# Kernel tuning notes

Measured on AMD Instinct MI355X. Metric: run time of the kernel, lower is better.

Reference implementation:

```python
import jax, jax.numpy as jnp
import numpy as np
import math

HEAD_DIM = 64
HEAD_NUM = 8  # hidden_dim(512) // head_dim(64)
EPS = 1e-8


def modulated_linear(x, s, weight, aff_w, aff_b):
    # x: [B, N, IN], s: [B, S], weight: [OUT, IN], aff_w: [IN, S], aff_b: [IN]
    style = s @ aff_w.T + aff_b                       # [B, IN]
    w = weight[None, :, :] * style[:, None, :]        # [B, OUT, IN]
    demod = jax.lax.rsqrt(jnp.sum(w * w, axis=2) + EPS)  # [B, OUT]
    w = w * demod[:, :, None]
    return jnp.einsum('bni,boi->bno', x, w)           # [B, N, OUT]


def setup_inputs() -> dict:
    key = jax.random.key(0)
    ks = jax.random.split(key, 8)
    B, N, F, S = 8, 1024, 512, 512
    sc = 1.0 / math.sqrt(F)
    return {
        'x': jax.random.normal(ks[0], (B, N, F), dtype=jnp.float32),
        's': jax.random.normal(ks[1], (B, S), dtype=jnp.float32),
        'k_weight': jax.random.normal(ks[2], (F, F), dtype=jnp.float32) * sc,
        'k_aff_w': jax.random.normal(ks[3], (F, S), dtype=jnp.float32) * sc,
        'k_aff_b': jnp.ones((F,), dtype=jnp.float32),
        'o_weight': jax.random.normal(ks[4], (F, F), dtype=jnp.float32) * sc,
        'o_aff_w': jax.random.normal(ks[5], (F, S), dtype=jnp.float32) * sc,
        'o_aff_b': jnp.ones((F,), dtype=jnp.float32),
    }


def reference(x, s, k_weight, k_aff_w, k_aff_b, o_weight, o_aff_w, o_aff_b):
    B, N, _ = x.shape
    # Original code computes q, k, v all via k_mapping (faithful to the bug).
    kqv = modulated_linear(x, s, k_weight, k_aff_w, k_aff_b)  # [B, N, hidden]
    kqv = kqv.reshape(B, N, HEAD_NUM, HEAD_DIM)               # [B, N, H, D]
    q = k = v = kqv
    scale = 1.0 / math.sqrt(HEAD_DIM)
    scores = jnp.einsum('bnhd,bmhd->bhnm', q, k) * scale      # [B, H, N, N]
    attn = jax.nn.softmax(scores, axis=-1)
    out = jnp.einsum('bhnm,bmhd->bnhd', attn, v)              # [B, N, H, D]
    out = out.reshape(B, N, HEAD_NUM * HEAD_DIM)
    return modulated_linear(out, s, o_weight, o_aff_w, o_aff_b)
```

## Files before the change

### kernel.cpp

```cpp
#include <hip/hip_runtime.h>
#include <stdint.h>

using short8  = __attribute__((ext_vector_type(8))) short;
using f32x4   = __attribute__((ext_vector_type(4))) float;
using float4v = __attribute__((ext_vector_type(4))) float;
using u16x4   = __attribute__((ext_vector_type(4))) unsigned short;

__device__ __forceinline__ unsigned short f2b(float f) {
    union { float f; unsigned int i; } v; v.f = f;
    unsigned int i = v.i;
    unsigned int r = (i + 0x7fffu + ((i >> 16) & 1u)) >> 16;
    return (unsigned short)r;
}
__device__ __forceinline__ short8 ld8(const unsigned short* p) {
    return *reinterpret_cast<const short8*>(p);
}
__device__ __forceinline__ void st8(unsigned short* p, short8 v) {
    *reinterpret_cast<short8*>(p) = v;
}
__device__ __forceinline__ short8 ldA(const unsigned short* p) { return ld8(p); }
__device__ __forceinline__ short8 ldA(const float* p) {
    float4v v0 = *reinterpret_cast<const float4v*>(p);
    float4v v1 = *reinterpret_cast<const float4v*>(p + 4);
    short8 o;
#pragma unroll
    for (int j = 0; j < 4; ++j) o[j] = (short)f2b(v0[j]);
#pragma unroll
    for (int j = 0; j < 4; ++j) o[4 + j] = (short)f2b(v1[j]);
    return o;
}
__device__ __forceinline__ f32x4 mfma16(short8 a, short8 b, f32x4 c) {
    return __builtin_amdgcn_mfma_f32_16x16x32_bf16(a, b, c, 0, 0, 0);
}
__device__ __forceinline__ void stC(float* p, float v)          { *p = v; }
__device__ __forceinline__ void stC(unsigned short* p, float v) { *p = f2b(v); }

__device__ __forceinline__ unsigned int cvtpk(float lo, float hi) {
    unsigned int r;
    asm("v_cvt_pk_bf16_f32 %0, %1, %2" : "=v"(r) : "v"(lo), "v"(hi));
    return r;
}
__device__ __forceinline__ void pl32swap(unsigned int& a, unsigned int& b) {
    asm("v_permlane32_swap_b32 %0, %1" : "+v"(a), "+v"(b));
}
__device__ __forceinline__ void pl16swap(unsigned int& a, unsigned int& b) {
    asm("v_permlane16_swap_b32 %0, %1" : "+v"(a), "+v"(b));
}
__device__ __forceinline__ short8 pack4(unsigned int x0, unsigned int x1,
                                        unsigned int x2, unsigned int x3) {
    union { unsigned int u[4]; short8 s; } c;
    c.u[0] = x0; c.u[1] = x1; c.u[2] = x2; c.u[3] = x3;
    return c.s;
}

__global__ __launch_bounds__(256) void style_kernel(
    const float* __restrict__ s,
    const float* __restrict__ k_aff_w, const float* __restrict__ k_aff_b,
    const float* __restrict__ o_aff_w, const float* __restrict__ o_aff_b,
    float* __restrict__ style)
{
    int wid  = blockIdx.x * 4 + (threadIdx.x >> 6);
    int lane = threadIdx.x & 63;
    int map  = wid >> 12;
    int rem  = wid & 4095;
    int b    = rem >> 9;
    int i    = rem & 511;
    const float* aw = map ? o_aff_w : k_aff_w;
    const float* ab = map ? o_aff_b : k_aff_b;
    const float* sp = s  + b * 512 + lane * 8;
    const float* wp = aw + i * 512 + lane * 8;
    float acc = 0.f;
#pragma unroll
    for (int j = 0; j < 8; ++j) acc += sp[j] * wp[j];
#pragma unroll
    for (int off = 1; off < 64; off <<= 1) acc += __shfl_xor(acc, off, 64);
    if (lane == 0) style[(map * 8 + b) * 512 + i] = acc + ab[i];
}

__global__ __launch_bounds__(256) void modw_kernel(
    const float* __restrict__ k_weight,
    const float* __restrict__ o_weight,
    const float* __restrict__ style,
    unsigned short* __restrict__ wmod)
{
    int wid  = blockIdx.x * 4 + (threadIdx.x >> 6);
    int lane = threadIdx.x & 63;
    int map  = wid >> 12;
    int rem  = wid & 4095;
    int b    = rem >> 9;
    int o    = rem & 511;
    const float* wrow = (map ? o_weight : k_weight) + o * 512 + lane * 8;
    const float* st   = style + (map * 8 + b) * 512 + lane * 8;
    float w[8]; float ss = 0.f;
#pragma unroll
    for (int j = 0; j < 8; ++j) { w[j] = wrow[j] * st[j]; ss += w[j] * w[j]; }
#pragma unroll
    for (int off = 1; off < 64; off <<= 1) ss += __shfl_xor(ss, off, 64);
    float demod = rsqrtf(ss + 1e-8f);
    short8 ov;
#pragma unroll
    for (int j = 0; j < 8; ++j) ov[j] = (short)f2b(w[j] * demod);
    unsigned short* dst = wmod + (((size_t)map * 8 + b) * 512 + o) * 512 + lane * 8;
    *reinterpret_cast<short8*>(dst) = ov;
}

template <typename AT, typename CT, bool WVT>
__global__ __launch_bounds__(256) void gemm_bt_lds_kernel(
    const AT* __restrict__ A,
    const unsigned short* __restrict__ Bt,
    CT* __restrict__ C,
    unsigned short* __restrict__ VT)
{
    constexpr int KP = 72;
    constexpr int TP = 72;
    __shared__ __align__(16) unsigned short smem[4 * 64 * KP];
    typedef unsigned short Plane[64][KP];
    Plane* As = reinterpret_cast<Plane*>(smem);
    Plane* Bs = reinterpret_cast<Plane*>(smem + 2 * 64 * KP);

    int blk = blockIdx.x;
    int b   = blk & 7;
    int rem = blk >> 3;
    int mt  = rem & 15;
    int nt  = rem >> 4;
    int tid  = threadIdx.x;
    int w    = tid >> 6;
    int lane = tid & 63;
    int quad = lane >> 4;
    int r    = lane & 15;
    int wm   = w >> 1;
    int wn   = w & 1;

    const AT*             Ab = A  + ((size_t)b * 1024 + mt * 64) * 512;
    const unsigned short* Bb = Bt + ((size_t)b * 512  + nt * 64) * 512;

    int srow = tid >> 2;
    int scol = (tid & 3) * 8;
    const AT*             ga = Ab + (size_t)srow * 512 + scol;
    const unsigned short* gb = Bb + (size_t)srow * 512 + scol;

    f32x4 acc[2][2];
#pragma unroll
    for (int i = 0; i < 2; ++i)
#pragma unroll
        for (int j = 0; j < 2; ++j) acc[i][j] = f32x4{0.f, 0.f, 0.f, 0.f};

    short8 rg[2][4];

    st8(&As[0][srow][scol],      ldA(ga));
    st8(&As[0][srow][scol + 32], ldA(ga + 32));
    st8(&Bs[0][srow][scol],      ld8(gb));
    st8(&Bs[0][srow][scol + 32], ld8(gb + 32));
    rg[1][0] = ldA(ga + 64);  rg[1][1] = ldA(ga + 96);
    rg[1][2] = ld8(gb + 64);  rg[1][3] = ld8(gb + 96);
    __syncthreads();

#pragma unroll
    for (int ks = 0; ks < 8; ++ks) {
        int s = ks & 1;
        if (ks < 6) {
            int ko = (ks + 2) * 64;
            rg[s][0] = ldA(ga + ko);       rg[s][1] = ldA(ga + ko + 32);
            rg[s][2] = ld8(gb + ko);       rg[s][3] = ld8(gb + ko + 32);
        }
#pragma unroll
        for (int kh = 0; kh < 2; ++kh) {
            short8 af[2], bf[2];
#pragma unroll
            for (int i = 0; i < 2; ++i)
                af[i] = ld8(&As[s][wm * 32 + i * 16 + r][kh * 32 + quad * 8]);
#pragma unroll
            for (int j = 0; j < 2; ++j)
                bf[j] = ld8(&Bs[s][wn * 32 + j * 16 + r][kh * 32 + quad * 8]);
#pragma unroll
            for (int i = 0; i < 2; ++i)
#pragma unroll
                for (int j = 0; j < 2; ++j)
                    acc[i][j] = mfma16(af[i], bf[j], acc[i][j]);
        }
        if (ks < 7) {
            int ns = s ^ 1;
            st8(&As[ns][srow][scol],      rg[ns][0]);
            st8(&As[ns][srow][scol + 32], rg[ns][1]);
            st8(&Bs[ns][srow][scol],      rg[ns][2]);
            st8(&Bs[ns][srow][scol + 32], rg[ns][3]);
        }
        __syncthreads();
    }

    CT* Cb = C + (size_t)b * 1024 * 512;
#pragma unroll
    for (int i = 0; i < 2; ++i)
#pragma unroll
        for (int rr = 0; rr < 4; ++rr) {
            int row = mt * 64 + wm * 32 + i * 16 + quad * 4 + rr;
#pragma unroll
            for (int j = 0; j < 2; ++j) {
                int col = nt * 64 + wn * 32 + j * 16 + r;
                stC(Cb + (size_t)row * 512 + col, acc[i][j][rr]);
            }
        }
    if (WVT) {
        unsigned short (*Tt)[TP] = reinterpret_cast<unsigned short (*)[TP]>(smem);
#pragma unroll
        for (int i = 0; i < 2; ++i)
#pragma unroll
            for (int j = 0; j < 2; ++j) {
                int d = wn * 32 + j * 16 + r;
#pragma unroll
                for (int rh = 0; rh < 2; ++rh) {
                    int tok = wm * 32 + i * 16 + quad * 4 + rh * 2;
                    unsigned int pv = (unsigned int)f2b(acc[i][j][rh * 2]) |
                                      ((unsigned int)f2b(acc[i][j][rh * 2 + 1]) << 16);
                    *reinterpret_cast<unsigned int*>(&Tt[d][tok]) = pv;
                }
            }
        __syncthreads();
        int d  = tid >> 2;
        int cc = tid & 3;
        const unsigned short* src = &Tt[d][cc * 16];
        unsigned short* dst = VT + ((size_t)(b * 8 + nt) * 64 + d) * 1024 + mt * 64 + cc * 16;
        short8 t0 = ld8(src), t1 = ld8(src + 8);
        st8(dst,     t0);
        st8(dst + 8, t1);
    }
}

__global__ __launch_bounds__(256) void attn_kernel(
    const unsigned short* __restrict__ kqv,
    const unsigned short* __restrict__ vt,
    unsigned short* __restrict__ attn_out)
{
    constexpr int PAD = 72;
    int blk = blockIdx.x;
    int bh = blk & 63;
    int qt = blk >> 6;
    int b  = bh >> 3, h = bh & 7;
    int tid  = threadIdx.x;
    int lane = tid & 63;
    int quad = lane >> 4;
    int r    = lane & 15;

    __shared__ __align__(16) unsigned short klds[2][64][PAD];
    __shared__ __align__(16) unsigned short vlds[2][64][PAD];

    const unsigned short* Mb = kqv + (size_t)b * 1024 * 512;
    int wv = tid >> 6;
    int q0 = qt * 64 + wv * 16;

    const unsigned short* qptr = Mb + (size_t)(q0 + r) * 512 + h * 64 + quad * 8;
    short8 bq0 = ld8(qptr);
    short8 bq1 = ld8(qptr + 32);

    short8 ones;
#pragma unroll
    for (int j = 0; j < 8; ++j) ones[j] = (short)0x3F80;

    f32x4 o0 = {0.f, 0.f, 0.f, 0.f};
    f32x4 o1 = o0, o2 = o0, o3 = o0, lacc = o0;

    int srow0 = tid >> 3;
    int srow1 = srow0 + 32;
    int scol  = (tid & 7) * 8;
    const unsigned short* Kg = Mb + h * 64;
    const unsigned short* Vg = vt + (size_t)bh * 64 * 1024;

    {
        short8 k0v = ld8(Kg + (size_t)srow0 * 512 + scol);
        short8 k1v = ld8(Kg + (size_t)srow1 * 512 + scol);
        short8 v0v = ld8(Vg + (size_t)srow0 * 1024 + scol);
        short8 v1v = ld8(Vg + (size_t)srow1 * 1024 + scol);
        st8(&klds[0][srow0][scol], k0v);
        st8(&klds[0][srow1][scol], k1v);
        st8(&vlds[0][srow0][scol], v0v);
        st8(&vlds[0][srow1][scol], v1v);
    }
    __syncthreads();

    const float c  = 0.18033688011112042f;
    const float CM = 28.853900817779268f;

    for (int it = 0; it < 16; ++it) {
        int s = it & 1;
        short8 pk0, pk1, pv0, pv1;
        if (it < 15) {
            int k0n = (it + 1) * 64;
            pk0 = ld8(Kg + (size_t)(k0n + srow0) * 512 + scol);
            pk1 = ld8(Kg + (size_t)(k0n + srow1) * 512 + scol);
            pv0 = ld8(Vg + (size_t)srow0 * 1024 + k0n + scol);
            pv1 = ld8(Vg + (size_t)srow1 * 1024 + k0n + scol);
        }
        f32x4 st_[4];
#pragma unroll
        for (int t = 0; t < 4; ++t) {
            short8 ka = ld8(&klds[s][t * 16 + r][quad * 8]);
            short8 kb = ld8(&klds[s][t * 16 + r][32 + quad * 8]);
            f32x4 sacc = {0.f, 0.f, 0.f, 0.f};
            sacc = mfma16(ka, bq0, sacc);
            sacc = mfma16(kb, bq1, sacc);
            st_[t] = sacc;
        }
        unsigned int pk_[4][2];
#pragma unroll
        for (int t = 0; t < 4; ++t)
#pragma unroll
            for (int h2 = 0; h2 < 2; ++h2)
                pk_[t][h2] = cvtpk(exp2f(st_[t][2 * h2]     * c - CM),
                                   exp2f(st_[t][2 * h2 + 1] * c - CM));
        unsigned int a0 = pk_[0][0], b0 = pk_[1][0];
        pl32swap(a0, b0); pl16swap(a0, b0);
        unsigned int a1 = pk_[0][1], b1 = pk_[1][1];
        pl32swap(a1, b1); pl16swap(a1, b1);
        unsigned int c0 = pk_[2][0], d0 = pk_[3][0];
        pl32swap(c0, d0); pl16swap(c0, d0);
        unsigned int c1 = pk_[2][1], d1 = pk_[3][1];
        pl32swap(c1, d1); pl16swap(c1, d1);
        short8 ap0 = pack4(a0, a1, b0, b1);
        short8 ap1 = pack4(c0, c1, d0, d1);
        {
            short8 va, vb;
            va = ld8(&vlds[s][0 * 16 + r][quad * 8]);
            vb = ld8(&vlds[s][0 * 16 + r][32 + quad * 8]);
            o0 = mfma16(ap0, va, o0);  o0 = mfma16(ap1, vb, o0);
            va = ld8(&vlds[s][1 * 16 + r][quad * 8]);
            vb = ld8(&vlds[s][1 * 16 + r][32 + quad * 8]);
            o1 = mfma16(ap0, va, o1);  o1 = mfma16(ap1, vb, o1);
            va = ld8(&vlds[s][2 * 16 + r][quad * 8]);
            vb = ld8(&vlds[s][2 * 16 + r][32 + quad * 8]);
            o2 = mfma16(ap0, va, o2);  o2 = mfma16(ap1, vb, o2);
            va = ld8(&vlds[s][3 * 16 + r][quad * 8]);
            vb = ld8(&vlds[s][3 * 16 + r][32 + quad * 8]);
            o3 = mfma16(ap0, va, o3);  o3 = mfma16(ap1, vb, o3);
            lacc = mfma16(ap0, ones, lacc);
            lacc = mfma16(ap1, ones, lacc);
        }
        if (it < 15) {
            int ns = s ^ 1;
            st8(&klds[ns][srow0][scol], pk0);
            st8(&klds[ns][srow1][scol], pk1);
            st8(&vlds[ns][srow0][scol], pv0);
            st8(&vlds[ns][srow1][scol], pv1);
        }
        __syncthreads();
    }

    unsigned short* ob = attn_out + (size_t)b * 1024 * 512 + (size_t)h * 64;
#pragma unroll
    for (int rr = 0; rr < 4; ++rr) {
        float inv = 1.0f / lacc[rr];
        int n = q0 + quad * 4 + rr;
        unsigned short* orow = ob + (size_t)n * 512 + r;
        orow[0]  = f2b(o0[rr] * inv);
        orow[16] = f2b(o1[rr] * inv);
        orow[32] = f2b(o2[rr] * inv);
        orow[48] = f2b(o3[rr] * inv);
    }
}

extern "C" void kernel_launch(void* const* d_in, const int* in_sizes, int n_in,
                              void* d_out, int out_size, void* d_ws, size_t ws_size,
                              hipStream_t stream)
{
    const float* x        = (const float*)d_in[0];
    const float* s        = (const float*)d_in[1];
    const float* k_weight = (const float*)d_in[2];
    const float* k_aff_w  = (const float*)d_in[3];
    const float* k_aff_b  = (const float*)d_in[4];
    const float* o_weight = (const float*)d_in[5];
    const float* o_aff_w  = (const float*)d_in[6];
    const float* o_aff_b  = (const float*)d_in[7];
    float* out = (float*)d_out;

    char* ws = (char*)d_ws;
    float* style          = (float*)ws;
    unsigned short* wmod  = (unsigned short*)(ws + 32 * 1024);
    unsigned short* attn  = wmod + (size_t)2 * 8 * 512 * 512;
    unsigned short* kqv   = attn + (size_t)8 * 1024 * 512;
    unsigned short* vt    = kqv  + (size_t)8 * 1024 * 512;

    style_kernel<<<2048, 256, 0, stream>>>(s, k_aff_w, k_aff_b, o_aff_w, o_aff_b, style);
    modw_kernel<<<2048, 256, 0, stream>>>(k_weight, o_weight, style, wmod);
    gemm_bt_lds_kernel<float, unsigned short, true><<<1024, 256, 0, stream>>>(x, wmod, kqv, vt);
    attn_kernel<<<1024, 256, 0, stream>>>(kqv, vt, attn);
    gemm_bt_lds_kernel<unsigned short, float, false><<<1024, 256, 0, stream>>>(attn, wmod + (size_t)8 * 512 * 512, out, nullptr);
}
```

Baseline: 139.9 us.

## Stage GEMM tiles with direct global-to-LDS loads and pre-convert x to bf16

Adds a separate kernel that converts x from fp32 to bf16 before the first GEMM. Both GEMMs now stage A and B tiles with global_load_lds straight into an XOR-swizzled, unpadded LDS layout, replacing the register round-trip and manual LDS stores. The aim is to cut VGPR pressure and VALU conversion work in the GEMM inner loop and to avoid LDS bank conflicts. In exchange it adds an extra kernel launch plus a full write and read of the bf16 copy of x, and the prefetch depth drops from two stages to one.

```diff
diff --git a/kernel.cpp b/kernel.cpp
--- a/kernel.cpp
+++ b/kernel.cpp
@@ -18,22 +18,18 @@
 __device__ __forceinline__ void st8(unsigned short* p, short8 v) {
     *reinterpret_cast<short8*>(p) = v;
 }
-__device__ __forceinline__ short8 ldA(const unsigned short* p) { return ld8(p); }
-__device__ __forceinline__ short8 ldA(const float* p) {
-    float4v v0 = *reinterpret_cast<const float4v*>(p);
-    float4v v1 = *reinterpret_cast<const float4v*>(p + 4);
-    short8 o;
-#pragma unroll
-    for (int j = 0; j < 4; ++j) o[j] = (short)f2b(v0[j]);
-#pragma unroll
-    for (int j = 0; j < 4; ++j) o[4 + j] = (short)f2b(v1[j]);
-    return o;
-}
 __device__ __forceinline__ f32x4 mfma16(short8 a, short8 b, f32x4 c) {
     return __builtin_amdgcn_mfma_f32_16x16x32_bf16(a, b, c, 0, 0, 0);
 }
 __device__ __forceinline__ void stC(float* p, float v)          { *p = v; }
 __device__ __forceinline__ void stC(unsigned short* p, float v) { *p = f2b(v); }
+
+__device__ __forceinline__ void gl16(const unsigned short* g, unsigned short* l) {
+    __builtin_amdgcn_global_load_lds(
+        (const __attribute__((address_space(1))) void*)g,
+        (__attribute__((address_space(3))) void*)l,
+        16, 0, 0);
+}
 
 __device__ __forceinline__ unsigned int cvtpk(float lo, float hi) {
     unsigned int r;
@@ -51,6 +47,20 @@
     union { unsigned int u[4]; short8 s; } c;
     c.u[0] = x0; c.u[1] = x1; c.u[2] = x2; c.u[3] = x3;
     return c.s;
+}
+
+__global__ __launch_bounds__(256) void cvt_kernel(
+    const float* __restrict__ x, unsigned short* __restrict__ xb)
+{
+    int i = (blockIdx.x * 256 + threadIdx.x) * 8;
+    float4v v0 = *reinterpret_cast<const float4v*>(x + i);
+    float4v v1 = *reinterpret_cast<const float4v*>(x + i + 4);
+    short8 o;
+#pragma unroll
+    for (int j = 0; j < 4; ++j) o[j] = (short)f2b(v0[j]);
+#pragma unroll
+    for (int j = 0; j < 4; ++j) o[4 + j] = (short)f2b(v1[j]);
+    st8(xb + i, o);
 }
 
 __global__ __launch_bounds__(256) void style_kernel(
@@ -104,19 +114,14 @@
     *reinterpret_cast<short8*>(dst) = ov;
 }
 
-template <typename AT, typename CT, bool WVT>
+template <typename CT, bool WVT>
 __global__ __launch_bounds__(256) void gemm_bt_lds_kernel(
-    const AT* __restrict__ A,
+    const unsigned short* __restrict__ A,
     const unsigned short* __restrict__ Bt,
     CT* __restrict__ C,
     unsigned short* __restrict__ VT)
 {
-    constexpr int KP = 72;
-    constexpr int TP = 72;
-    __shared__ __align__(16) unsigned short smem[4 * 64 * KP];
-    typedef unsigned short Plane[64][KP];
-    Plane* As = reinterpret_cast<Plane*>(smem);
-    Plane* Bs = reinterpret_cast<Plane*>(smem + 2 * 64 * KP);
+    __shared__ __align__(16) unsigned short smem[4 * 4096];
 
     int blk = blockIdx.x;
     int b   = blk & 7;
@@ -131,13 +136,12 @@
     int wm   = w >> 1;
     int wn   = w & 1;
 
-    const AT*             Ab = A  + ((size_t)b * 1024 + mt * 64) * 512;
+    const unsigned short* Ab = A  + ((size_t)b * 1024 + mt * 64) * 512;
     const unsigned short* Bb = Bt + ((size_t)b * 512  + nt * 64) * 512;
 
-    int srow = tid >> 2;
-    int scol = (tid & 3) * 8;
-    const AT*             ga = Ab + (size_t)srow * 512 + scol;
-    const unsigned short* gb = Bb + (size_t)srow * 512 + scol;
+    int lrow = lane >> 3;
+    int lunit = (lane & 7) ^ lrow;
+    int laneoff = lrow * 512 + lunit * 8;
 
     f32x4 acc[2][2];
 #pragma unroll
@@ -145,45 +149,44 @@
 #pragma unroll
         for (int j = 0; j < 2; ++j) acc[i][j] = f32x4{0.f, 0.f, 0.f, 0.f};
 
-    short8 rg[2][4];
-
-    st8(&As[0][srow][scol],      ldA(ga));
-    st8(&As[0][srow][scol + 32], ldA(ga + 32));
-    st8(&Bs[0][srow][scol],      ld8(gb));
-    st8(&Bs[0][srow][scol + 32], ld8(gb + 32));
-    rg[1][0] = ldA(ga + 64);  rg[1][1] = ldA(ga + 96);
-    rg[1][2] = ld8(gb + 64);  rg[1][3] = ld8(gb + 96);
+    auto stage = [&](int sbuf, int kt) {
+        int ko = kt * 64;
+        unsigned short* Asb = smem + sbuf * 4096;
+        unsigned short* Bsb = smem + 8192 + sbuf * 4096;
+#pragma unroll
+        for (int c = 0; c < 2; ++c) {
+            int chunk = w * 2 + c;
+            gl16(Ab + (size_t)chunk * 8 * 512 + laneoff + ko, Asb + chunk * 512);
+            gl16(Bb + (size_t)chunk * 8 * 512 + laneoff + ko, Bsb + chunk * 512);
+        }
+    };
+    auto frag = [&](int row, int kh) {
+        return row * 64 + ((((kh << 2) | quad) ^ (row & 7)) << 3);
+    };
+
+    stage(0, 0);
     __syncthreads();
 
 #pragma unroll
     for (int ks = 0; ks < 8; ++ks) {
         int s = ks & 1;
-        if (ks < 6) {
-            int ko = (ks + 2) * 64;
-            rg[s][0] = ldA(ga + ko);       rg[s][1] = ldA(ga + ko + 32);
-            rg[s][2] = ld8(gb + ko);       rg[s][3] = ld8(gb + ko + 32);
-        }
+        if (ks < 7) stage(s ^ 1, ks + 1);
+        const unsigned short* Ap = smem + s * 4096;
+        const unsigned short* Bp = smem + 8192 + s * 4096;
 #pragma unroll
         for (int kh = 0; kh < 2; ++kh) {
             short8 af[2], bf[2];
 #pragma unroll
             for (int i = 0; i < 2; ++i)
-                af[i] = ld8(&As[s][wm * 32 + i * 16 + r][kh * 32 + quad * 8]);
+                af[i] = ld8(Ap + frag(wm * 32 + i * 16 + r, kh));
 #pragma unroll
             for (int j = 0; j < 2; ++j)
-                bf[j] = ld8(&Bs[s][wn * 32 + j * 16 + r][kh * 32 + quad * 8]);
+                bf[j] = ld8(Bp + frag(wn * 32 + j * 16 + r, kh));
 #pragma unroll
             for (int i = 0; i < 2; ++i)
 #pragma unroll
                 for (int j = 0; j < 2; ++j)
                     acc[i][j] = mfma16(af[i], bf[j], acc[i][j]);
-        }
-        if (ks < 7) {
-            int ns = s ^ 1;
-            st8(&As[ns][srow][scol],      rg[ns][0]);
-            st8(&As[ns][srow][scol + 32], rg[ns][1]);
-            st8(&Bs[ns][srow][scol],      rg[ns][2]);
-            st8(&Bs[ns][srow][scol + 32], rg[ns][3]);
         }
         __syncthreads();
     }
@@ -201,6 +204,7 @@
             }
         }
     if (WVT) {
+        constexpr int TP = 72;
         unsigned short (*Tt)[TP] = reinterpret_cast<unsigned short (*)[TP]>(smem);
 #pragma unroll
         for (int i = 0; i < 2; ++i)
@@ -377,10 +381,12 @@
     unsigned short* attn  = wmod + (size_t)2 * 8 * 512 * 512;
     unsigned short* kqv   = attn + (size_t)8 * 1024 * 512;
     unsigned short* vt    = kqv  + (size_t)8 * 1024 * 512;
-
+    unsigned short* xb    = vt   + (size_t)64 * 64 * 1024;
+
+    cvt_kernel  <<<2048, 256, 0, stream>>>(x, xb);
     style_kernel<<<2048, 256, 0, stream>>>(s, k_aff_w, k_aff_b, o_aff_w, o_aff_b, style);
-    modw_kernel<<<2048, 256, 0, stream>>>(k_weight, o_weight, style, wmod);
-    gemm_bt_lds_kernel<float, unsigned short, true><<<1024, 256, 0, stream>>>(x, wmod, kqv, vt);
+    modw_kernel <<<2048, 256, 0, stream>>>(k_weight, o_weight, style, wmod);
+    gemm_bt_lds_kernel<unsigned short, true><<<1024, 256, 0, stream>>>(xb, wmod, kqv, vt);
     attn_kernel<<<1024, 256, 0, stream>>>(kqv, vt, attn);
-    gemm_bt_lds_kernel<unsigned short, float, false><<<1024, 256, 0, stream>>>(attn, wmod + (size_t)8 * 512 * 512, out, nullptr);
-}
+    gemm_bt_lds_kernel<float, false><<<1024, 256, 0, stream>>>(attn, wmod + (size_t)8 * 512 * 512, out, nullptr);
+}
```

Result: no change. 140.8 us (+0.7%).
